# Kernel tuning notes

Hardware: AMD Instinct MI355X
Metric: run time of the kernel (lower is better)

The kernel has to match this reference:

```python
import jax, jax.numpy as jnp
import numpy as np

WS = 7      # window size
NH = 8      # num heads

def setup_inputs() -> dict:
    key = jax.random.key(0)
    k1, k2, k3 = jax.random.split(key, 3)
    B, H, W, C = 32, 56, 56, 256
    x = jax.random.normal(k1, (B, H, W, C), dtype=jnp.float32)
    w_qkv = jax.random.normal(k2, (3 * C, C), dtype=jnp.float32) * 0.02
    w_proj = jax.random.normal(k3, (C, C), dtype=jnp.float32) * 0.02
    b_proj = jnp.zeros((C,), dtype=jnp.float32)
    return {"x": x, "w_qkv": w_qkv, "w_proj": w_proj, "b_proj": b_proj}

def reference(x, w_qkv, w_proj, b_proj):
    B, H, W, C = x.shape
    hd = C // NH
    scale = hd ** -0.5
    # window partition: (B,H,W,C) -> (nW, ws^2, C)
    xw = x.reshape(B, H // WS, WS, W // WS, WS, C)
    xw = xw.transpose(0, 1, 3, 2, 4, 5).reshape(-1, WS * WS, C)
    # fused qkv projection (no bias)
    qkv = (xw @ w_qkv.T).reshape(-1, WS * WS, 3, NH, hd)
    q, k, v = qkv[:, :, 0], qkv[:, :, 1], qkv[:, :, 2]  # (nW, ws^2, nh, hd)
    # NOTE: faithful to source quirk — contraction over head_dim per token,
    # producing an (nh x nh) head-mixing attention matrix per token.
    attn = jnp.einsum('nshd,nsed->nshe', q, k) * scale   # (nW, ws^2, nh, nh)
    attn = jax.nn.softmax(attn, axis=-1)
    out = jnp.einsum('nshe,nsed->nshd', attn, v)         # (nW, ws^2, nh, hd)
    # source does transpose(1,2).reshape(-1, ws^2, C) — replicate exactly
    out = out.swapaxes(1, 2).reshape(-1, WS * WS, C)
    out = out @ w_proj.T + b_proj
    # window un-partition
    out = out.reshape(B, H // WS, W // WS, WS, WS, C)
    out = out.transpose(0, 1, 3, 2, 4, 5).reshape(B, H, W, C)
    return out
```

## Files before the change

kernel.cpp:

```cpp
#include <hip/hip_runtime.h>
#include <hip/hip_bf16.h>

typedef __bf16 bf16_t;
typedef bf16_t bf16x8 __attribute__((ext_vector_type(8)));
typedef float floatx4 __attribute__((ext_vector_type(4)));

#define MFMA16(a, b, c) __builtin_amdgcn_mfma_f32_16x16x32_bf16((a), (b), (c), 0, 0, 0)

__global__ __launch_bounds__(256) void wconv_kernel(
    const float* __restrict__ w_qkv, const float* __restrict__ w_proj,
    bf16_t* __restrict__ wb)
{
  int i = blockIdx.x * 256 + threadIdx.x;
  const float* src;
  bf16_t* dst;
  if (i < 24576) {
    int chunk = i >> 6, l = i & 63;
    int c = chunk >> 3, k = chunk & 7;
    int col = c * 16 + (l & 15);
    int kk = k * 32 + (l >> 4) * 8;
    src = w_qkv + col * 256 + kk;
    dst = wb + (i << 3);
  } else {
    int ip = i - 24576;
    int chunk = ip >> 6, l = ip & 63;
    int p = chunk >> 4, rem = chunk & 15, k = rem >> 1, j = rem & 1;
    int col = p * 32 + j * 16 + (l & 15);
    int kk = k * 32 + (l >> 4) * 8;
    src = w_proj + col * 256 + kk;
    dst = wb + 196608 + (ip << 3);
  }
  float4 f0 = ((const float4*)src)[0];
  float4 f1 = ((const float4*)src)[1];
  bf16_t t8[8] = {(bf16_t)f0.x, (bf16_t)f0.y, (bf16_t)f0.z, (bf16_t)f0.w,
                  (bf16_t)f1.x, (bf16_t)f1.y, (bf16_t)f1.z, (bf16_t)f1.w};
  *(uint4*)dst = *(const uint4*)t8;
}

__device__ __forceinline__ void cvt8_store(bf16_t* dst, float4 f0, float4 f1) {
  bf16_t t8[8] = {(bf16_t)f0.x, (bf16_t)f0.y, (bf16_t)f0.z, (bf16_t)f0.w,
                  (bf16_t)f1.x, (bf16_t)f1.y, (bf16_t)f1.z, (bf16_t)f1.w};
  *(uint4*)dst = *(const uint4*)t8;
}

#define XS_S 264
#define QK_S 520

__global__ __launch_bounds__(512, 4) void attn_kernel(
    const float* __restrict__ x,
    const bf16_t* __restrict__ wb,
    float* __restrict__ outf,
    bf16_t* __restrict__ preb)
{
  __shared__ __align__(16) bf16_t Xs[32][XS_S];
  __shared__ __align__(16) bf16_t QK[32][QK_S];
  __shared__ __align__(16) _Float16 Pl[32][8][8];

  const int tid = threadIdx.x;
  const int wave = tid >> 6, lane = tid & 63, quad = lane >> 4, l16 = lane & 15;
  const long base = (long)blockIdx.x * 32;
  const float scale = 0.17677669529663687f;

  const float* xb = x + base * 256;
#pragma unroll
  for (int it = 0; it < 2; ++it) {
    int idx = tid + it * 512;
    int s = idx >> 5, g = (idx & 31) * 8;
    const float* p = xb + s * 256 + g;
    float4 f0 = ((const float4*)p)[0];
    float4 f1 = ((const float4*)p)[1];
    cvt8_store(&Xs[s][g], f0, f1);
  }
  __syncthreads();

  floatx4 acc[2][6];
#pragma unroll
  for (int i = 0; i < 2; ++i)
#pragma unroll
    for (int j = 0; j < 6; ++j) acc[i][j] = (floatx4){0.f, 0.f, 0.f, 0.f};
  {
    auto loadB6 = [&](bf16x8 (&dst)[6], int k) {
      const bf16_t* cb = wb + ((long)(wave * 48 + k) << 9) + lane * 8;
#pragma unroll
      for (int j = 0; j < 6; ++j) dst[j] = *(const bf16x8*)(cb + (j << 12));
    };
    bf16x8 Ba[6], Bb[6];
    loadB6(Ba, 0);
#pragma unroll
    for (int k = 0; k < 8; ++k) {
      const bf16x8* cur = (k & 1) ? Bb : Ba;
      if (k < 7) loadB6((k & 1) ? Ba : Bb, k + 1);
      bf16x8 A0 = *(const bf16x8*)(&Xs[l16][k * 32 + quad * 8]);
      bf16x8 A1 = *(const bf16x8*)(&Xs[16 + l16][k * 32 + quad * 8]);
#pragma unroll
      for (int j = 0; j < 6; ++j) {
        acc[0][j] = MFMA16(A0, cur[j], acc[0][j]);
        acc[1][j] = MFMA16(A1, cur[j], acc[1][j]);
      }
    }
  }
  __syncthreads();

#pragma unroll
  for (int j = 0; j < 6; ++j) {
    int g = wave * 96 + j * 16 + l16;
#pragma unroll
    for (int i = 0; i < 2; ++i)
#pragma unroll
      for (int r = 0; r < 4; ++r) {
        int row = i * 16 + quad * 4 + r;
        if (g < 512) QK[row][g] = (bf16_t)acc[i][j][r];
        else         Xs[row][g - 512] = (bf16_t)acc[i][j][r];
      }
  }
  __syncthreads();

  {
    const int t = tid >> 4, h = (tid >> 1) & 7, sg = tid & 1;
    const bf16_t* qrow = &QK[t][h * 32 + sg * 16];
    float qf[16];
    {
      bf16x8 q0 = *(const bf16x8*)(qrow);
      bf16x8 q1 = *(const bf16x8*)(qrow + 8);
#pragma unroll
      for (int d = 0; d < 8; ++d) { qf[d] = (float)q0[d]; qf[8 + d] = (float)q1[d]; }
    }
    float sc[8];
#pragma unroll
    for (int e = 0; e < 8; ++e) {
      const bf16_t* krow = &QK[t][256 + e * 32 + sg * 16];
      bf16x8 k0 = *(const bf16x8*)(krow);
      bf16x8 k1 = *(const bf16x8*)(krow + 8);
      float a = 0.f;
#pragma unroll
      for (int d = 0; d < 8; ++d) a += qf[d] * (float)k0[d] + qf[8 + d] * (float)k1[d];
      sc[e] = a;
    }
#pragma unroll
    for (int e = 0; e < 8; ++e) sc[e] += __shfl_xor(sc[e], 1);
    float mx = -INFINITY;
#pragma unroll
    for (int e = 0; e < 8; ++e) { sc[e] *= scale; mx = fmaxf(mx, sc[e]); }
    float sum = 0.f, pv[8];
#pragma unroll
    for (int e = 0; e < 8; ++e) { pv[e] = __expf(sc[e] - mx); sum += pv[e]; }
    float rs = 1.0f / sum;
    if (sg == 0) {
      _Float16 ph[8];
#pragma unroll
      for (int e = 0; e < 8; ++e) ph[e] = (_Float16)(pv[e] * rs);
      *(uint4*)(&Pl[t][h][0]) = *(const uint4*)ph;
    }
  }
  __syncthreads();

  {
    const int t = tid >> 4, j = tid & 15, j8 = j & 7, h0 = j >> 3;
    float pf[4][8];
#pragma unroll
    for (int m = 0; m < 4; ++m) {
      _Float16 ph[8];
      *(uint4*)ph = *(const uint4*)(&Pl[t][h0 + 2 * m][0]);
#pragma unroll
      for (int e = 0; e < 8; ++e) pf[m][e] = (float)ph[e];
    }
    float pr[4][4];
#pragma unroll
    for (int m = 0; m < 4; ++m)
#pragma unroll
      for (int d = 0; d < 4; ++d) pr[m][d] = 0.f;
#pragma unroll
    for (int e = 0; e < 8; ++e) {
      bf16_t v4[4];
      *(uint2*)v4 = *(const uint2*)(&Xs[t][e * 32 + j8 * 4]);
      float vf[4];
#pragma unroll
      for (int d = 0; d < 4; ++d) vf[d] = (float)v4[d];
#pragma unroll
      for (int m = 0; m < 4; ++m) {
        float pe = pf[m][e];
#pragma unroll
        for (int d = 0; d < 4; ++d) pr[m][d] += pe * vf[d];
      }
    }
    if (preb) {
      bf16_t* op = preb + (base + t) * 256 + j * 4;
#pragma unroll
      for (int m = 0; m < 4; ++m) {
        bf16_t o4[4] = {(bf16_t)pr[m][0], (bf16_t)pr[m][1],
                        (bf16_t)pr[m][2], (bf16_t)pr[m][3]};
        *(uint2*)(op + m * 64) = *(const uint2*)o4;
      }
    } else {
      float* op = outf + (base + t) * 256 + j * 4;
#pragma unroll
      for (int m = 0; m < 4; ++m) {
        float4 f = {pr[m][0], pr[m][1], pr[m][2], pr[m][3]};
        *(float4*)(op + m * 64) = f;
      }
    }
  }
}

__global__ __launch_bounds__(512, 4) void proj_kernel(
    const bf16_t* __restrict__ wb,
    const float* __restrict__ b_proj,
    float* __restrict__ out,
    const bf16_t* __restrict__ preb)
{
  const int n = blockIdx.x;
  const int b = n >> 6, wh = (n >> 3) & 7, ww = n & 7;
  const int rowbase = b * 3136 + wh * 392 + ww * 7;
  const int tid = threadIdx.x;
  const int wave = tid >> 6, lane = tid & 63, quad = lane >> 4, l16 = lane & 15;

  auto loadBp = [&](bf16x8 (&dst)[2], int k) {
#pragma unroll
    for (int j = 0; j < 2; ++j)
      dst[j] = *(const bf16x8*)(wb + 196608 +
          ((long)(wave * 16 + k * 2 + j) << 9) + lane * 8);
  };
  auto loadA = [&](bf16x8 (&dst)[4], int k) {
#pragma unroll
    for (int i = 0; i < 4; ++i) {
      int mr = i * 16 + l16; if (mr > 48) mr = 48;
      int q5 = mr * 8 + k;
      int h = q5 / 49;
      int s = q5 - h * 49;
      int srow = (s / 7) * 56 + (s - (s / 7) * 7);
      dst[i] = *(const bf16x8*)(preb + (long)(rowbase + srow) * 256 +
                                h * 32 + quad * 8);
    }
  };

  const float bv0 = b_proj[wave * 32 + l16];
  const float bv1 = b_proj[wave * 32 + 16 + l16];

  floatx4 acc[4][2];
#pragma unroll
  for (int i = 0; i < 4; ++i)
#pragma unroll
    for (int j = 0; j < 2; ++j) acc[i][j] = (floatx4){0.f, 0.f, 0.f, 0.f};

  bf16x8 Aa[4], Ab[4], Ba[2], Bb[2];
  loadA(Aa, 0); loadBp(Ba, 0);
#pragma unroll
  for (int k = 0; k < 8; ++k) {
    const bf16x8* cA = (k & 1) ? Ab : Aa;
    const bf16x8* cB = (k & 1) ? Bb : Ba;
    if (k < 7) { loadA((k & 1) ? Aa : Ab, k + 1); loadBp((k & 1) ? Ba : Bb, k + 1); }
#pragma unroll
    for (int i = 0; i < 4; ++i) {
      acc[i][0] = MFMA16(cA[i], cB[0], acc[i][0]);
      acc[i][1] = MFMA16(cA[i], cB[1], acc[i][1]);
    }
  }
#pragma unroll
  for (int i = 0; i < 4; ++i)
#pragma unroll
    for (int r = 0; r < 4; ++r) {
      int m = i * 16 + quad * 4 + r;
      if (m < 49) {
        int srow = (m / 7) * 56 + (m - (m / 7) * 7);
        float* orow = out + (long)(rowbase + srow) * 256 + wave * 32 + l16;
        orow[0]  = acc[i][0][r] + bv0;
        orow[16] = acc[i][1][r] + bv1;
      }
    }
}

#define SC_S 264
__global__ __launch_bounds__(512, 4) void proj_fallback(
    const bf16_t* __restrict__ wb,
    const float* __restrict__ b_proj,
    float* out)
{
  __shared__ __align__(16) bf16_t Sc[49][SC_S];
  __shared__ int trow[49];
  const int n = blockIdx.x;
  const int b = n >> 6, wh = (n >> 3) & 7, ww = n & 7;
  const int tid = threadIdx.x;
  const int wave = tid >> 6, lane = tid & 63, quad = lane >> 4, l16 = lane & 15;

  auto loadBp = [&](bf16x8 (&dst)[2], int k) {
#pragma unroll
    for (int j = 0; j < 2; ++j)
      dst[j] = *(const bf16x8*)(wb + 196608 +
          ((long)(wave * 16 + k * 2 + j) << 9) + lane * 8);
  };
  const float bv0 = b_proj[wave * 32 + l16];
  const float bv1 = b_proj[wave * 32 + 16 + l16];

  if (tid < 49) {
    int i = tid / 7, j = tid % 7;
    trow[tid] = b * 3136 + (wh * 7 + i) * 56 + ww * 7 + j;
  }
  __syncthreads();
  for (int idx = tid; idx < 49 * 32; idx += 512) {
    int s = idx >> 5, c8 = idx & 31;
    const float* p = out + (long)trow[s] * 256 + c8 * 8;
    float4 f0 = ((const float4*)p)[0];
    float4 f1 = ((const float4*)p)[1];
    int flat = (c8 >> 2) * 1568 + s * 32 + (c8 & 3) * 8;
    cvt8_store(&Sc[flat >> 8][flat & 255], f0, f1);
  }
  __syncthreads();
  floatx4 acc[4][2];
#pragma unroll
  for (int i = 0; i < 4; ++i)
#pragma unroll
    for (int j = 0; j < 2; ++j) acc[i][j] = (floatx4){0.f, 0.f, 0.f, 0.f};
  bf16x8 Aa[4], Ab[4], Ba[2], Bb[2];
  auto loadA = [&](bf16x8* dst, int k) {
#pragma unroll
    for (int i = 0; i < 4; ++i) {
      int mr = i * 16 + l16; if (mr > 48) mr = 48;
      dst[i] = *(const bf16x8*)(&Sc[mr][k * 32 + quad * 8]);
    }
  };
  loadA(Aa, 0); loadBp(Ba, 0);
#pragma unroll
  for (int k = 0; k < 8; ++k) {
    const bf16x8* cA = (k & 1) ? Ab : Aa;
    const bf16x8* cB = (k & 1) ? Bb : Ba;
    if (k < 7) { loadA((k & 1) ? Aa : Ab, k + 1); loadBp((k & 1) ? Ba : Bb, k + 1); }
#pragma unroll
    for (int i = 0; i < 4; ++i) {
      acc[i][0] = MFMA16(cA[i], cB[0], acc[i][0]);
      acc[i][1] = MFMA16(cA[i], cB[1], acc[i][1]);
    }
  }
#pragma unroll
  for (int i = 0; i < 4; ++i)
#pragma unroll
    for (int r = 0; r < 4; ++r) {
      int m = i * 16 + quad * 4 + r;
      if (m < 49) {
        float* orow = out + (long)trow[m] * 256 + wave * 32 + l16;
        orow[0]  = acc[i][0][r] + bv0;
        orow[16] = acc[i][1][r] + bv1;
      }
    }
}

extern "C" void kernel_launch(void* const* d_in, const int* in_sizes, int n_in,
                              void* d_out, int out_size, void* d_ws, size_t ws_size,
                              hipStream_t stream) {
  (void)in_sizes; (void)n_in; (void)out_size;
  const float* x      = (const float*)d_in[0];
  const float* w_qkv  = (const float*)d_in[1];
  const float* w_proj = (const float*)d_in[2];
  const float* b_proj = (const float*)d_in[3];
  float* out = (float*)d_out;
  bf16_t* wb = (bf16_t*)d_ws;

  bf16_t* preb = nullptr;
  if (ws_size >= (size_t)524288 + 51380224) preb = wb + 262144;

  wconv_kernel<<<dim3(128), 256, 0, stream>>>(w_qkv, w_proj, wb);
  attn_kernel<<<dim3(3136), 512, 0, stream>>>(x, wb, out, preb);
  if (preb)
    proj_kernel<<<dim3(2048), 512, 0, stream>>>(wb, b_proj, out, preb);
  else
    proj_fallback<<<dim3(2048), 512, 0, stream>>>(wb, b_proj, out);
}
```

Before: 293.7 us.

## Fuse QKV, head-mixing attention and output projection into one per-window kernel

Replaces the separate attention kernel (32-token tiles) and projection kernel with a single kernel that processes one 49-token window per block. The QKV GEMM runs in two M passes, V is written into the reused X buffer, and the softmax probabilities and the head-scrambled attention output are staged in shared memory. The projection GEMM then reads that tile directly from shared memory. This removes the bf16 intermediate round-trip through global memory and one kernel launch. In exchange it uses more shared memory per block, which may reduce occupancy, and about a quarter of the MFMA rows in the two-pass QKV GEMM are padding.

```diff
diff --git a/kernel.cpp b/kernel.cpp
--- a/kernel.cpp
+++ b/kernel.cpp
@@ -46,307 +46,240 @@
 #define XS_S 264
 #define QK_S 520
 
-__global__ __launch_bounds__(512, 4) void attn_kernel(
+__global__ __launch_bounds__(512, 4) void fused_kernel(
     const float* __restrict__ x,
     const bf16_t* __restrict__ wb,
-    float* __restrict__ outf,
-    bf16_t* __restrict__ preb)
+    const float* __restrict__ b_proj,
+    float* __restrict__ out)
 {
-  __shared__ __align__(16) bf16_t Xs[32][XS_S];
-  __shared__ __align__(16) bf16_t QK[32][QK_S];
-  __shared__ __align__(16) _Float16 Pl[32][8][8];
-
-  const int tid = threadIdx.x;
-  const int wave = tid >> 6, lane = tid & 63, quad = lane >> 4, l16 = lane & 15;
-  const long base = (long)blockIdx.x * 32;
-  const float scale = 0.17677669529663687f;
-
-  const float* xb = x + base * 256;
-#pragma unroll
-  for (int it = 0; it < 2; ++it) {
-    int idx = tid + it * 512;
-    int s = idx >> 5, g = (idx & 31) * 8;
-    const float* p = xb + s * 256 + g;
-    float4 f0 = ((const float4*)p)[0];
-    float4 f1 = ((const float4*)p)[1];
-    cvt8_store(&Xs[s][g], f0, f1);
-  }
-  __syncthreads();
-
-  floatx4 acc[2][6];
-#pragma unroll
-  for (int i = 0; i < 2; ++i)
-#pragma unroll
-    for (int j = 0; j < 6; ++j) acc[i][j] = (floatx4){0.f, 0.f, 0.f, 0.f};
-  {
-    auto loadB6 = [&](bf16x8 (&dst)[6], int k) {
-      const bf16_t* cb = wb + ((long)(wave * 48 + k) << 9) + lane * 8;
-#pragma unroll
-      for (int j = 0; j < 6; ++j) dst[j] = *(const bf16x8*)(cb + (j << 12));
-    };
-    bf16x8 Ba[6], Bb[6];
-    loadB6(Ba, 0);
-#pragma unroll
-    for (int k = 0; k < 8; ++k) {
-      const bf16x8* cur = (k & 1) ? Bb : Ba;
-      if (k < 7) loadB6((k & 1) ? Ba : Bb, k + 1);
-      bf16x8 A0 = *(const bf16x8*)(&Xs[l16][k * 32 + quad * 8]);
-      bf16x8 A1 = *(const bf16x8*)(&Xs[16 + l16][k * 32 + quad * 8]);
-#pragma unroll
-      for (int j = 0; j < 6; ++j) {
-        acc[0][j] = MFMA16(A0, cur[j], acc[0][j]);
-        acc[1][j] = MFMA16(A1, cur[j], acc[1][j]);
-      }
-    }
-  }
-  __syncthreads();
-
-#pragma unroll
-  for (int j = 0; j < 6; ++j) {
-    int g = wave * 96 + j * 16 + l16;
-#pragma unroll
-    for (int i = 0; i < 2; ++i)
-#pragma unroll
-      for (int r = 0; r < 4; ++r) {
-        int row = i * 16 + quad * 4 + r;
-        if (g < 512) QK[row][g] = (bf16_t)acc[i][j][r];
-        else         Xs[row][g - 512] = (bf16_t)acc[i][j][r];
-      }
-  }
-  __syncthreads();
-
-  {
-    const int t = tid >> 4, h = (tid >> 1) & 7, sg = tid & 1;
-    const bf16_t* qrow = &QK[t][h * 32 + sg * 16];
-    float qf[16];
-    {
-      bf16x8 q0 = *(const bf16x8*)(qrow);
-      bf16x8 q1 = *(const bf16x8*)(qrow + 8);
-#pragma unroll
-      for (int d = 0; d < 8; ++d) { qf[d] = (float)q0[d]; qf[8 + d] = (float)q1[d]; }
-    }
-    float sc[8];
-#pragma unroll
-    for (int e = 0; e < 8; ++e) {
-      const bf16_t* krow = &QK[t][256 + e * 32 + sg * 16];
-      bf16x8 k0 = *(const bf16x8*)(krow);
-      bf16x8 k1 = *(const bf16x8*)(krow + 8);
-      float a = 0.f;
-#pragma unroll
-      for (int d = 0; d < 8; ++d) a += qf[d] * (float)k0[d] + qf[8 + d] * (float)k1[d];
-      sc[e] = a;
-    }
-#pragma unroll
-    for (int e = 0; e < 8; ++e) sc[e] += __shfl_xor(sc[e], 1);
-    float mx = -INFINITY;
-#pragma unroll
-    for (int e = 0; e < 8; ++e) { sc[e] *= scale; mx = fmaxf(mx, sc[e]); }
-    float sum = 0.f, pv[8];
-#pragma unroll
-    for (int e = 0; e < 8; ++e) { pv[e] = __expf(sc[e] - mx); sum += pv[e]; }
-    float rs = 1.0f / sum;
-    if (sg == 0) {
-      _Float16 ph[8];
-#pragma unroll
-      for (int e = 0; e < 8; ++e) ph[e] = (_Float16)(pv[e] * rs);
-      *(uint4*)(&Pl[t][h][0]) = *(const uint4*)ph;
-    }
-  }
-  __syncthreads();
-
-  {
-    const int t = tid >> 4, j = tid & 15, j8 = j & 7, h0 = j >> 3;
-    float pf[4][8];
-#pragma unroll
-    for (int m = 0; m < 4; ++m) {
-      _Float16 ph[8];
-      *(uint4*)ph = *(const uint4*)(&Pl[t][h0 + 2 * m][0]);
-#pragma unroll
-      for (int e = 0; e < 8; ++e) pf[m][e] = (float)ph[e];
-    }
-    float pr[4][4];
-#pragma unroll
-    for (int m = 0; m < 4; ++m)
-#pragma unroll
-      for (int d = 0; d < 4; ++d) pr[m][d] = 0.f;
-#pragma unroll
-    for (int e = 0; e < 8; ++e) {
-      bf16_t v4[4];
-      *(uint2*)v4 = *(const uint2*)(&Xs[t][e * 32 + j8 * 4]);
-      float vf[4];
-#pragma unroll
-      for (int d = 0; d < 4; ++d) vf[d] = (float)v4[d];
-#pragma unroll
-      for (int m = 0; m < 4; ++m) {
-        float pe = pf[m][e];
-#pragma unroll
-        for (int d = 0; d < 4; ++d) pr[m][d] += pe * vf[d];
-      }
-    }
-    if (preb) {
-      bf16_t* op = preb + (base + t) * 256 + j * 4;
-#pragma unroll
-      for (int m = 0; m < 4; ++m) {
-        bf16_t o4[4] = {(bf16_t)pr[m][0], (bf16_t)pr[m][1],
-                        (bf16_t)pr[m][2], (bf16_t)pr[m][3]};
-        *(uint2*)(op + m * 64) = *(const uint2*)o4;
-      }
-    } else {
-      float* op = outf + (base + t) * 256 + j * 4;
-#pragma unroll
-      for (int m = 0; m < 4; ++m) {
-        float4 f = {pr[m][0], pr[m][1], pr[m][2], pr[m][3]};
-        *(float4*)(op + m * 64) = f;
-      }
-    }
-  }
-}
-
-__global__ __launch_bounds__(512, 4) void proj_kernel(
-    const bf16_t* __restrict__ wb,
-    const float* __restrict__ b_proj,
-    float* __restrict__ out,
-    const bf16_t* __restrict__ preb)
-{
+  __shared__ __align__(16) bf16_t Xs[49][XS_S];
+  __shared__ __align__(16) bf16_t QK[49][QK_S];
+
   const int n = blockIdx.x;
   const int b = n >> 6, wh = (n >> 3) & 7, ww = n & 7;
   const int rowbase = b * 3136 + wh * 392 + ww * 7;
   const int tid = threadIdx.x;
   const int wave = tid >> 6, lane = tid & 63, quad = lane >> 4, l16 = lane & 15;
-
-  auto loadBp = [&](bf16x8 (&dst)[2], int k) {
-#pragma unroll
-    for (int j = 0; j < 2; ++j)
-      dst[j] = *(const bf16x8*)(wb + 196608 +
-          ((long)(wave * 16 + k * 2 + j) << 9) + lane * 8);
-  };
-  auto loadA = [&](bf16x8 (&dst)[4], int k) {
-#pragma unroll
-    for (int i = 0; i < 4; ++i) {
-      int mr = i * 16 + l16; if (mr > 48) mr = 48;
-      int q5 = mr * 8 + k;
-      int h = q5 / 49;
-      int s = q5 - h * 49;
-      int srow = (s / 7) * 56 + (s - (s / 7) * 7);
-      dst[i] = *(const bf16x8*)(preb + (long)(rowbase + srow) * 256 +
-                                h * 32 + quad * 8);
-    }
-  };
+  const float scale = 0.17677669529663687f;
 
   const float bv0 = b_proj[wave * 32 + l16];
   const float bv1 = b_proj[wave * 32 + 16 + l16];
 
-  floatx4 acc[4][2];
-#pragma unroll
-  for (int i = 0; i < 4; ++i)
-#pragma unroll
-    for (int j = 0; j < 2; ++j) acc[i][j] = (floatx4){0.f, 0.f, 0.f, 0.f};
-
-  bf16x8 Aa[4], Ab[4], Ba[2], Bb[2];
-  loadA(Aa, 0); loadBp(Ba, 0);
-#pragma unroll
-  for (int k = 0; k < 8; ++k) {
-    const bf16x8* cA = (k & 1) ? Ab : Aa;
-    const bf16x8* cB = (k & 1) ? Bb : Ba;
-    if (k < 7) { loadA((k & 1) ? Aa : Ab, k + 1); loadBp((k & 1) ? Ba : Bb, k + 1); }
-#pragma unroll
-    for (int i = 0; i < 4; ++i) {
-      acc[i][0] = MFMA16(cA[i], cB[0], acc[i][0]);
-      acc[i][1] = MFMA16(cA[i], cB[1], acc[i][1]);
-    }
-  }
-#pragma unroll
-  for (int i = 0; i < 4; ++i)
-#pragma unroll
-    for (int r = 0; r < 4; ++r) {
-      int m = i * 16 + quad * 4 + r;
-      if (m < 49) {
-        int srow = (m / 7) * 56 + (m - (m / 7) * 7);
-        float* orow = out + (long)(rowbase + srow) * 256 + wave * 32 + l16;
-        orow[0]  = acc[i][0][r] + bv0;
-        orow[16] = acc[i][1][r] + bv1;
-      }
-    }
-}
-
-#define SC_S 264
-__global__ __launch_bounds__(512, 4) void proj_fallback(
-    const bf16_t* __restrict__ wb,
-    const float* __restrict__ b_proj,
-    float* out)
-{
-  __shared__ __align__(16) bf16_t Sc[49][SC_S];
-  __shared__ int trow[49];
-  const int n = blockIdx.x;
-  const int b = n >> 6, wh = (n >> 3) & 7, ww = n & 7;
-  const int tid = threadIdx.x;
-  const int wave = tid >> 6, lane = tid & 63, quad = lane >> 4, l16 = lane & 15;
-
-  auto loadBp = [&](bf16x8 (&dst)[2], int k) {
-#pragma unroll
-    for (int j = 0; j < 2; ++j)
-      dst[j] = *(const bf16x8*)(wb + 196608 +
-          ((long)(wave * 16 + k * 2 + j) << 9) + lane * 8);
-  };
-  const float bv0 = b_proj[wave * 32 + l16];
-  const float bv1 = b_proj[wave * 32 + 16 + l16];
-
-  if (tid < 49) {
-    int i = tid / 7, j = tid % 7;
-    trow[tid] = b * 3136 + (wh * 7 + i) * 56 + ww * 7 + j;
-  }
-  __syncthreads();
-  for (int idx = tid; idx < 49 * 32; idx += 512) {
-    int s = idx >> 5, c8 = idx & 31;
-    const float* p = out + (long)trow[s] * 256 + c8 * 8;
+  for (int idx = tid; idx < 1568; idx += 512) {
+    int s = idx >> 5, g = (idx & 31) * 8;
+    int srow = (s / 7) * 56 + (s % 7);
+    const float* p = x + (long)(rowbase + srow) * 256 + g;
     float4 f0 = ((const float4*)p)[0];
     float4 f1 = ((const float4*)p)[1];
-    int flat = (c8 >> 2) * 1568 + s * 32 + (c8 & 3) * 8;
-    cvt8_store(&Sc[flat >> 8][flat & 255], f0, f1);
-  }
-  __syncthreads();
-  floatx4 acc[4][2];
-#pragma unroll
-  for (int i = 0; i < 4; ++i)
-#pragma unroll
-    for (int j = 0; j < 2; ++j) acc[i][j] = (floatx4){0.f, 0.f, 0.f, 0.f};
-  bf16x8 Aa[4], Ab[4], Ba[2], Bb[2];
-  auto loadA = [&](bf16x8* dst, int k) {
-#pragma unroll
-    for (int i = 0; i < 4; ++i) {
-      int mr = i * 16 + l16; if (mr > 48) mr = 48;
-      dst[i] = *(const bf16x8*)(&Sc[mr][k * 32 + quad * 8]);
-    }
-  };
-  loadA(Aa, 0); loadBp(Ba, 0);
-#pragma unroll
-  for (int k = 0; k < 8; ++k) {
-    const bf16x8* cA = (k & 1) ? Ab : Aa;
-    const bf16x8* cB = (k & 1) ? Bb : Ba;
-    if (k < 7) { loadA((k & 1) ? Aa : Ab, k + 1); loadBp((k & 1) ? Ba : Bb, k + 1); }
-#pragma unroll
-    for (int i = 0; i < 4; ++i) {
-      acc[i][0] = MFMA16(cA[i], cB[0], acc[i][0]);
-      acc[i][1] = MFMA16(cA[i], cB[1], acc[i][1]);
-    }
-  }
-#pragma unroll
-  for (int i = 0; i < 4; ++i)
-#pragma unroll
-    for (int r = 0; r < 4; ++r) {
-      int m = i * 16 + quad * 4 + r;
-      if (m < 49) {
-        float* orow = out + (long)trow[m] * 256 + wave * 32 + l16;
-        orow[0]  = acc[i][0][r] + bv0;
-        orow[16] = acc[i][1][r] + bv1;
-      }
-    }
+    cvt8_store(&Xs[s][g], f0, f1);
+  }
+  __syncthreads();
+
+  auto loadB6 = [&](bf16x8 (&dst)[6], int k) {
+    const bf16_t* cb = wb + ((long)(wave * 48 + k) << 9) + lane * 8;
+#pragma unroll
+    for (int j = 0; j < 6; ++j) dst[j] = *(const bf16x8*)(cb + (j << 12));
+  };
+
+  floatx4 acc[2][6];
+  auto run_pass = [&](int mp) {
+#pragma unroll
+    for (int i = 0; i < 2; ++i)
+#pragma unroll
+      for (int j = 0; j < 6; ++j) acc[i][j] = (floatx4){0.f, 0.f, 0.f, 0.f};
+    bf16x8 Ba[6], Bb[6];
+    loadB6(Ba, 0);
+#pragma unroll
+    for (int k = 0; k < 8; ++k) {
+      const bf16x8* cur = (k & 1) ? Bb : Ba;
+      if (k < 7) loadB6((k & 1) ? Ba : Bb, k + 1);
+      int r0 = mp * 32 + l16;
+      int r1 = r0 + 16; if (r1 > 48) r1 = 48;
+      bf16x8 A0 = *(const bf16x8*)(&Xs[r0][k * 32 + quad * 8]);
+      bf16x8 A1 = *(const bf16x8*)(&Xs[r1][k * 32 + quad * 8]);
+#pragma unroll
+      for (int j = 0; j < 6; ++j) {
+        acc[0][j] = MFMA16(A0, cur[j], acc[0][j]);
+        acc[1][j] = MFMA16(A1, cur[j], acc[1][j]);
+      }
+    }
+  };
+  auto writeQK = [&](int mp) {
+#pragma unroll
+    for (int j = 0; j < 6; ++j) {
+      int g = wave * 96 + j * 16 + l16;
+      if (g < 512) {
+#pragma unroll
+        for (int i = 0; i < 2; ++i)
+#pragma unroll
+          for (int r = 0; r < 4; ++r) {
+            int row = (mp * 2 + i) * 16 + quad * 4 + r;
+            if (row < 49) QK[row][g] = (bf16_t)acc[i][j][r];
+          }
+      }
+    }
+  };
+  auto writeV = [&](int mp) {
+#pragma unroll
+    for (int j = 0; j < 6; ++j) {
+      int g = wave * 96 + j * 16 + l16;
+      if (g >= 512) {
+#pragma unroll
+        for (int i = 0; i < 2; ++i)
+#pragma unroll
+          for (int r = 0; r < 4; ++r) {
+            int row = (mp * 2 + i) * 16 + quad * 4 + r;
+            if (row < 49) Xs[row][g - 512] = (bf16_t)acc[i][j][r];
+          }
+      }
+    }
+  };
+
+  run_pass(0);
+  writeQK(0);
+  __syncthreads();
+  writeV(0);
+  run_pass(1);
+  writeQK(1);
+  __syncthreads();
+  writeV(1);
+
+  const int s_ = tid >> 3, h_ = tid & 7;
+  const bool sm = (tid < 392);
+  float sc[8];
+  if (sm) {
+    float qf[32];
+#pragma unroll
+    for (int u = 0; u < 4; ++u) {
+      bf16x8 qv = *(const bf16x8*)(&QK[s_][h_ * 32 + u * 8]);
+#pragma unroll
+      for (int d = 0; d < 8; ++d) qf[u * 8 + d] = (float)qv[d];
+    }
+#pragma unroll
+    for (int e = 0; e < 8; ++e) {
+      bf16x8 k0 = *(const bf16x8*)(&QK[s_][256 + e * 32]);
+      bf16x8 k1 = *(const bf16x8*)(&QK[s_][256 + e * 32 + 8]);
+      bf16x8 k2 = *(const bf16x8*)(&QK[s_][256 + e * 32 + 16]);
+      bf16x8 k3 = *(const bf16x8*)(&QK[s_][256 + e * 32 + 24]);
+      float a = 0.f;
+#pragma unroll
+      for (int d = 0; d < 8; ++d)
+        a += qf[d] * (float)k0[d] + qf[8 + d] * (float)k1[d] +
+             qf[16 + d] * (float)k2[d] + qf[24 + d] * (float)k3[d];
+      sc[e] = a;
+    }
+    float mx = -INFINITY;
+#pragma unroll
+    for (int e = 0; e < 8; ++e) { sc[e] *= scale; mx = fmaxf(mx, sc[e]); }
+    float sum = 0.f;
+#pragma unroll
+    for (int e = 0; e < 8; ++e) { sc[e] = __expf(sc[e] - mx); sum += sc[e]; }
+    float rs = 1.0f / sum;
+#pragma unroll
+    for (int e = 0; e < 8; ++e) sc[e] *= rs;
+  }
+  __syncthreads();
+  if (sm) {
+    _Float16 ph[8];
+#pragma unroll
+    for (int e = 0; e < 8; ++e) ph[e] = (_Float16)sc[e];
+    *(uint4*)((_Float16*)&QK[s_][320] + h_ * 8) = *(const uint4*)ph;
+  }
+  __syncthreads();
+
+  auto pv_task = [&](int idx) {
+    int t = idx >> 4, j = idx & 15, j8 = j & 7, h0 = j >> 3;
+    float pf[4][8];
+#pragma unroll
+    for (int m = 0; m < 4; ++m) {
+      _Float16 ph[8];
+      *(uint4*)ph = *(const uint4*)((const _Float16*)&QK[t][320] + (h0 + 2 * m) * 8);
+#pragma unroll
+      for (int e = 0; e < 8; ++e) pf[m][e] = (float)ph[e];
+    }
+    float pr[4][4];
+#pragma unroll
+    for (int m = 0; m < 4; ++m)
+#pragma unroll
+      for (int d = 0; d < 4; ++d) pr[m][d] = 0.f;
+#pragma unroll
+    for (int e = 0; e < 8; ++e) {
+      bf16_t v4[4];
+      *(uint2*)v4 = *(const uint2*)(&Xs[t][e * 32 + j8 * 4]);
+      float vf[4];
+#pragma unroll
+      for (int d = 0; d < 4; ++d) vf[d] = (float)v4[d];
+#pragma unroll
+      for (int m = 0; m < 4; ++m) {
+        float pe = pf[m][e];
+#pragma unroll
+        for (int d = 0; d < 4; ++d) pr[m][d] += pe * vf[d];
+      }
+    }
+#pragma unroll
+    for (int m = 0; m < 4; ++m) {
+      int c = m * 64 + j * 4;
+      int flat = (c >> 5) * 1568 + t * 32 + (c & 31);
+      bf16_t o4[4] = {(bf16_t)pr[m][0], (bf16_t)pr[m][1],
+                      (bf16_t)pr[m][2], (bf16_t)pr[m][3]};
+      *(uint2*)(&QK[flat >> 8][flat & 255]) = *(const uint2*)o4;
+    }
+  };
+  pv_task(tid);
+  if (tid < 272) pv_task(tid + 512);
+  __syncthreads();
+
+  {
+    auto loadBp = [&](bf16x8 (&dst)[2], int k) {
+#pragma unroll
+      for (int j = 0; j < 2; ++j)
+        dst[j] = *(const bf16x8*)(wb + 196608 +
+            ((long)(wave * 16 + k * 2 + j) << 9) + lane * 8);
+    };
+    auto loadA = [&](bf16x8 (&dst)[4], int k) {
+#pragma unroll
+      for (int i = 0; i < 4; ++i) {
+        int mr = i * 16 + l16; if (mr > 48) mr = 48;
+        dst[i] = *(const bf16x8*)(&QK[mr][k * 32 + quad * 8]);
+      }
+    };
+    floatx4 pacc[4][2];
+#pragma unroll
+    for (int i = 0; i < 4; ++i)
+#pragma unroll
+      for (int j = 0; j < 2; ++j) pacc[i][j] = (floatx4){0.f, 0.f, 0.f, 0.f};
+    bf16x8 Aa[4], Ab[4], Ba[2], Bb[2];
+    loadA(Aa, 0); loadBp(Ba, 0);
+#pragma unroll
+    for (int k = 0; k < 8; ++k) {
+      const bf16x8* cA = (k & 1) ? Ab : Aa;
+      const bf16x8* cB = (k & 1) ? Bb : Ba;
+      if (k < 7) { loadA((k & 1) ? Aa : Ab, k + 1); loadBp((k & 1) ? Ba : Bb, k + 1); }
+#pragma unroll
+      for (int i = 0; i < 4; ++i) {
+        pacc[i][0] = MFMA16(cA[i], cB[0], pacc[i][0]);
+        pacc[i][1] = MFMA16(cA[i], cB[1], pacc[i][1]);
+      }
+    }
+#pragma unroll
+    for (int i = 0; i < 4; ++i)
+#pragma unroll
+      for (int r = 0; r < 4; ++r) {
+        int m = i * 16 + quad * 4 + r;
+        if (m < 49) {
+          int srow = (m / 7) * 56 + (m % 7);
+          float* orow = out + (long)(rowbase + srow) * 256 + wave * 32 + l16;
+          orow[0]  = pacc[i][0][r] + bv0;
+          orow[16] = pacc[i][1][r] + bv1;
+        }
+      }
+  }
 }
 
 extern "C" void kernel_launch(void* const* d_in, const int* in_sizes, int n_in,
                               void* d_out, int out_size, void* d_ws, size_t ws_size,
                               hipStream_t stream) {
-  (void)in_sizes; (void)n_in; (void)out_size;
+  (void)in_sizes; (void)n_in; (void)out_size; (void)ws_size;
   const float* x      = (const float*)d_in[0];
   const float* w_qkv  = (const float*)d_in[1];
   const float* w_proj = (const float*)d_in[2];
@@ -354,13 +287,6 @@
   float* out = (float*)d_out;
   bf16_t* wb = (bf16_t*)d_ws;
 
-  bf16_t* preb = nullptr;
-  if (ws_size >= (size_t)524288 + 51380224) preb = wb + 262144;
-
   wconv_kernel<<<dim3(128), 256, 0, stream>>>(w_qkv, w_proj, wb);
-  attn_kernel<<<dim3(3136), 512, 0, stream>>>(x, wb, out, preb);
-  if (preb)
-    proj_kernel<<<dim3(2048), 512, 0, stream>>>(wb, b_proj, out, preb);
-  else
-    proj_fallback<<<dim3(2048), 512, 0, stream>>>(wb, b_proj, out);
-}
+  fused_kernel<<<dim3(2048), 512, 0, stream>>>(x, wb, b_proj, out);
+}
```

Result: slower. 305.2 us (+3.9%).
